# Optimization experiments

Measured on AMD Instinct MI355X. Metric: run time of the kernel, lower is better.

The kernel has to match this reference:

```python
import jax, jax.numpy as jnp
import numpy as np

ALPHA = 0.2  # LeakyReLU negative slope
NEG_INF = -1e12


def setup_inputs() -> dict:
    key = jax.random.key(0)
    k1, k2, k3, k4, k5 = jax.random.split(key, 5)
    N, F = 4096, 512
    inp = jax.random.normal(k1, (N, F), dtype=jnp.float32)
    adj = jax.random.randint(k2, (N, N), 0, 2).astype(jnp.float32)
    W = jax.random.normal(k3, (F, F), dtype=jnp.float32) * (1.414 / np.sqrt(F))
    a = jax.random.normal(k4, (2 * F, 1), dtype=jnp.float32) * 0.05
    wtrans = jax.random.normal(k5, (2 * F, F), dtype=jnp.float32) * (1.414 / np.sqrt(1.5 * F))
    return {"inp": inp, "adj": adj, "W": W, "a": a, "wtrans": wtrans}


def reference(inp, adj, W, a, wtrans):
    F_out = W.shape[1]
    h = inp @ W                                   # [N, F]
    Wh1 = h @ a[:F_out, :]                        # [N, 1]
    Wh2 = h @ a[F_out:, :]                        # [N, 1]
    e = jax.nn.leaky_relu(Wh1 + Wh2.T, ALPHA)     # [N, N]
    mask = adj > 0
    attention = jax.nn.softmax(jnp.where(mask, e, NEG_INF), axis=1)
    negative_attention = -jax.nn.softmax(jnp.where(mask, -e, NEG_INF), axis=1)
    # dropout p=0.0 (eval mode): identity
    h_prime = attention @ inp                     # [N, F_in]
    h_prime_negative = negative_attention @ inp   # [N, F_in]
    h_prime_double = jnp.concatenate([h_prime, h_prime_negative], axis=1)
    new_h_prime = h_prime_double @ wtrans         # [N, F_out]
    return jax.nn.elu(new_h_prime)
```

## Files before the change

### kernel.cpp

```cpp
#include <hip/hip_runtime.h>
#include <hip/hip_bf16.h>

#define N_NODES 4096
#define F_DIM   512
#define KTOT    8192
#define KSPLIT  8
#define LOG2E   1.44269504f

typedef __attribute__((ext_vector_type(8))) short bf16x8;
typedef __attribute__((ext_vector_type(4))) float f32x4;

__device__ inline unsigned short f2bf(float f) {
  union { float f; unsigned u; } c; c.f = f;
  unsigned r = c.u + 0x7fffu + ((c.u >> 16) & 1u);
  return (unsigned short)(r >> 16);
}
__device__ inline float bf2f(unsigned short u) {
  union { unsigned u; float f; } c; c.u = ((unsigned)u) << 16;
  return c.f;
}

__global__ void k_compute_v(const float* __restrict__ W, const float* __restrict__ a,
                            float* __restrict__ v1, float* __restrict__ v2) {
  int r = blockIdx.x, l = threadIdx.x;
  float s1 = 0.f, s2 = 0.f;
  for (int c = l; c < F_DIM; c += 64) {
    float w = W[(size_t)r * F_DIM + c];
    s1 += w * a[c];
    s2 += w * a[F_DIM + c];
  }
#pragma unroll
  for (int off = 32; off > 0; off >>= 1) { s1 += __shfl_down(s1, off); s2 += __shfl_down(s2, off); }
  if (l == 0) { v1[r] = s1; v2[r] = s2; }
}

__global__ void k_compute_wh(const float* __restrict__ inp, const float* __restrict__ v1,
                             const float* __restrict__ v2, float* __restrict__ Wh1,
                             float* __restrict__ Wh2) {
  int i = blockIdx.x, l = threadIdx.x;
  float s1 = 0.f, s2 = 0.f;
  for (int c = l; c < F_DIM; c += 64) {
    float x = inp[(size_t)i * F_DIM + c];
    s1 += x * v1[c];
    s2 += x * v2[c];
  }
#pragma unroll
  for (int off = 32; off > 0; off >>= 1) { s1 += __shfl_down(s1, off); s2 += __shfl_down(s2, off); }
  if (l == 0) { Wh1[i] = s1 * LOG2E; Wh2[i] = s2 * LOG2E; }
}

__global__ void k_transpose_bf16(const float* __restrict__ src, unsigned short* __restrict__ dst,
                                 int R, int C) {
  __shared__ float tile[32][33];
  int c0 = blockIdx.x * 32, r0 = blockIdx.y * 32;
  int tx = threadIdx.x, ty = threadIdx.y;
#pragma unroll
  for (int i = ty; i < 32; i += 8)
    tile[i][tx] = src[(size_t)(r0 + i) * C + c0 + tx];
  __syncthreads();
#pragma unroll
  for (int i = ty; i < 32; i += 8)
    dst[(size_t)(c0 + i) * R + r0 + tx] = f2bf(tile[tx][i]);
}

__global__ __launch_bounds__(256) void k_y(const float* __restrict__ inp,
                                           const unsigned short* __restrict__ wtT,
                                           unsigned short* __restrict__ YT) {
  int tid = threadIdx.x, l = tid & 63, w = tid >> 6;
  int row = l & 15, kg = l >> 4;
  int jt = blockIdx.x * 64 + w * 16;
  int cb = blockIdx.y * 64;
  f32x4 acc1[4] = {}, acc2[4] = {};
  const float* ap = inp + (size_t)(jt + row) * F_DIM + kg * 8;
  for (int k0 = 0; k0 < F_DIM; k0 += 32) {
    float4 f0 = *(const float4*)(ap + k0);
    float4 f1 = *(const float4*)(ap + k0 + 4);
    bf16x8 a;
    a[0] = (short)f2bf(f0.x); a[1] = (short)f2bf(f0.y); a[2] = (short)f2bf(f0.z); a[3] = (short)f2bf(f0.w);
    a[4] = (short)f2bf(f1.x); a[5] = (short)f2bf(f1.y); a[6] = (short)f2bf(f1.z); a[7] = (short)f2bf(f1.w);
#pragma unroll
    for (int n = 0; n < 4; n++) {
      const unsigned short* bp = wtT + (size_t)(cb + n * 16 + row) * 1024 + kg * 8 + k0;
      bf16x8 b1 = *(const bf16x8*)(bp);
      bf16x8 b2 = *(const bf16x8*)(bp + F_DIM);
      acc1[n] = __builtin_amdgcn_mfma_f32_16x16x32_bf16(a, b1, acc1[n], 0, 0, 0);
      acc2[n] = __builtin_amdgcn_mfma_f32_16x16x32_bf16(a, b2, acc2[n], 0, 0, 0);
    }
  }
  int jb = jt + kg * 4;
#pragma unroll
  for (int n = 0; n < 4; n++) {
    int f = cb + n * 16 + row;
    ushort4 o1, o2;
    o1.x = f2bf(acc1[n][0]); o1.y = f2bf(acc1[n][1]); o1.z = f2bf(acc1[n][2]); o1.w = f2bf(acc1[n][3]);
    o2.x = f2bf(acc2[n][0]); o2.y = f2bf(acc2[n][1]); o2.z = f2bf(acc2[n][2]); o2.w = f2bf(acc2[n][3]);
    *(ushort4*)(YT + (size_t)f * KTOT + jb) = o1;
    *(ushort4*)(YT + (size_t)f * KTOT + 4096 + jb) = o2;
  }
}

__global__ __launch_bounds__(256) void k_p(const float* __restrict__ adj,
                                           const float* __restrict__ Wh1,
                                           const float* __restrict__ Wh2,
                                           unsigned short* __restrict__ Pcat) {
  int i = blockIdx.x, t = threadIdx.x;
  float w1 = Wh1[i];
  int j0 = t * 16;
  const float* ar = adj + (size_t)i * N_NODES + j0;
  float4 A0 = *(const float4*)(ar);
  float4 A1 = *(const float4*)(ar + 4);
  float4 A2 = *(const float4*)(ar + 8);
  float4 A3 = *(const float4*)(ar + 12);
  float am[16] = {A0.x, A0.y, A0.z, A0.w, A1.x, A1.y, A1.z, A1.w,
                  A2.x, A2.y, A2.z, A2.w, A3.x, A3.y, A3.z, A3.w};
  float4 wv0 = *(const float4*)(Wh2 + j0);
  float4 wv1 = *(const float4*)(Wh2 + j0 + 4);
  float4 wv2 = *(const float4*)(Wh2 + j0 + 8);
  float4 wv3 = *(const float4*)(Wh2 + j0 + 12);
  float w2[16] = {wv0.x, wv0.y, wv0.z, wv0.w, wv1.x, wv1.y, wv1.z, wv1.w,
                  wv2.x, wv2.y, wv2.z, wv2.w, wv3.x, wv3.y, wv3.z, wv3.w};
  float pe[16], ne[16];
  float sp = 0.f, sn = 0.f;
#pragma unroll
  for (int r = 0; r < 16; r++) {
    float s = w1 + w2[r];
    float e = fmaxf(s, 0.2f * s);
    float p = exp2f(e);
    float n = exp2f(-e);
    if (!(am[r] > 0.f)) { p = 0.f; n = 0.f; }
    pe[r] = p; ne[r] = n; sp += p; sn += n;
  }
#pragma unroll
  for (int off = 1; off < 64; off <<= 1) { sp += __shfl_xor(sp, off); sn += __shfl_xor(sn, off); }
  __shared__ float red[2][4];
  int wv = t >> 6, ln = t & 63;
  if (ln == 0) { red[0][wv] = sp; red[1][wv] = sn; }
  __syncthreads();
  sp = red[0][0] + red[0][1] + red[0][2] + red[0][3];
  sn = red[1][0] + red[1][1] + red[1][2] + red[1][3];
  float rp = 1.f / sp;
  float rn = -1.f / sn;
  bf16x8 o;
#pragma unroll
  for (int r = 0; r < 8; r++) o[r] = (short)f2bf(pe[r] * rp);
  *(bf16x8*)(Pcat + (size_t)i * KTOT + j0) = o;
#pragma unroll
  for (int r = 0; r < 8; r++) o[r] = (short)f2bf(pe[8 + r] * rp);
  *(bf16x8*)(Pcat + (size_t)i * KTOT + j0 + 8) = o;
#pragma unroll
  for (int r = 0; r < 8; r++) o[r] = (short)f2bf(ne[r] * rn);
  *(bf16x8*)(Pcat + (size_t)i * KTOT + 4096 + j0) = o;
#pragma unroll
  for (int r = 0; r < 8; r++) o[r] = (short)f2bf(ne[8 + r] * rn);
  *(bf16x8*)(Pcat + (size_t)i * KTOT + 4096 + j0 + 8) = o;
}

#define GLOAD16(gp, lp) __builtin_amdgcn_global_load_lds( \
    (const __attribute__((address_space(1))) unsigned int*)(gp), \
    (__attribute__((address_space(3))) unsigned int*)(lp), 16, 0, 0)

__global__ __launch_bounds__(512, 2) void k_pv(const unsigned short* __restrict__ Pcat,
                                               const unsigned short* __restrict__ YT,
                                               unsigned short* __restrict__ part) {
  __shared__ unsigned short Ab[3][256 * 32];
  __shared__ unsigned short Bb[3][256 * 32];
  const int kchunk = KTOT / KSPLIT;
  int t = threadIdx.x;
  int l = t & 63, w = t >> 6;
  int la = l & 15, kg = l >> 4;
  int wr = w >> 2, wc = w & 3;
  int bm0 = blockIdx.x * 256, bn0 = blockIdx.y * 256;
  size_t kbase = (size_t)blockIdx.z * kchunk;
  const int nsteps = kchunk / 32;

  int seg = ((t & 3) ^ ((t >> 3) & 3)) << 4;
  const char* gA = (const char*)Pcat + ((size_t)(bm0 + (t >> 2)) * KTOT + kbase) * 2 + seg;
  const char* gB = (const char*)YT   + ((size_t)(bn0 + (t >> 2)) * KTOT + kbase) * 2 + seg;
  const size_t rstep = (size_t)128 * KTOT * 2;

  int aswz = (kg ^ ((la >> 1) & 3)) << 4;
  int abase = (wr * 128 + la) * 64 + aswz;
  int bbase = (wc * 64 + la) * 64 + aswz;

  f32x4 acc[8][4] = {};

#define STAGE3(buf, st) do { \
    const char* _ga = gA + (size_t)(st) * 64; \
    const char* _gb = gB + (size_t)(st) * 64; \
    char* _la = (char*)&Ab[buf][0] + w * 1024; \
    char* _lb = (char*)&Bb[buf][0] + w * 1024; \
    GLOAD16(_ga, _la); \
    GLOAD16(_ga + rstep, _la + 8192); \
    GLOAD16(_gb, _lb); \
    GLOAD16(_gb + rstep, _lb + 8192); \
  } while (0)

  STAGE3(0, 0);
  STAGE3(1, 1);
  for (int st = 0; st < nsteps; st++) {
    __builtin_amdgcn_s_barrier();
    int buf = st % 3;
    if (st + 2 < nsteps) {
      STAGE3((st + 2) % 3, st + 2);
      asm volatile("s_waitcnt vmcnt(8)" ::: "memory");
    } else if (st + 1 < nsteps) {
      asm volatile("s_waitcnt vmcnt(4)" ::: "memory");
    } else {
      asm volatile("s_waitcnt vmcnt(0)" ::: "memory");
    }
    __builtin_amdgcn_s_barrier();

    const char* Abp = (const char*)&Ab[buf][0];
    const char* Bbp = (const char*)&Bb[buf][0];
    bf16x8 af[8], bfr[4];
#pragma unroll
    for (int mi = 0; mi < 8; mi++) af[mi] = *(const bf16x8*)(Abp + abase + mi * 1024);
#pragma unroll
    for (int ni = 0; ni < 4; ni++) bfr[ni] = *(const bf16x8*)(Bbp + bbase + ni * 1024);
    __builtin_amdgcn_s_setprio(1);
#pragma unroll
    for (int mi = 0; mi < 8; mi++)
#pragma unroll
      for (int ni = 0; ni < 4; ni++)
        acc[mi][ni] = __builtin_amdgcn_mfma_f32_16x16x32_bf16(af[mi], bfr[ni], acc[mi][ni], 0, 0, 0);
    __builtin_amdgcn_s_setprio(0);
  }

  unsigned short* po = part + (size_t)blockIdx.z * (N_NODES * F_DIM);
#pragma unroll
  for (int mi = 0; mi < 8; mi++)
#pragma unroll
    for (int ni = 0; ni < 4; ni++)
#pragma unroll
      for (int r = 0; r < 4; r++) {
        int i_ = bm0 + wr * 128 + mi * 16 + kg * 4 + r;
        int f_ = bn0 + wc * 64 + ni * 16 + la;
        po[(size_t)i_ * F_DIM + f_] = f2bf(acc[mi][ni][r]);
      }
}

__global__ __launch_bounds__(256) void k_fin(const unsigned short* __restrict__ part,
                                             float* __restrict__ out) {
  size_t idx = ((size_t)blockIdx.x * 256 + threadIdx.x) * 8;
  float s[8] = {};
#pragma unroll
  for (int p = 0; p < KSPLIT; p++) {
    bf16x8 v = *(const bf16x8*)(part + (size_t)p * (N_NODES * F_DIM) + idx);
#pragma unroll
    for (int r = 0; r < 8; r++) s[r] += bf2f((unsigned short)v[r]);
  }
#pragma unroll
  for (int r = 0; r < 8; r++) s[r] = s[r] > 0.f ? s[r] : (__expf(s[r]) - 1.f);
  float4 o0 = make_float4(s[0], s[1], s[2], s[3]);
  float4 o1 = make_float4(s[4], s[5], s[6], s[7]);
  *(float4*)(out + idx) = o0;
  *(float4*)(out + idx + 4) = o1;
}

extern "C" void kernel_launch(void* const* d_in, const int* in_sizes, int n_in,
                              void* d_out, int out_size, void* d_ws, size_t ws_size,
                              hipStream_t stream) {
  (void)in_sizes; (void)n_in; (void)out_size; (void)ws_size;
  const float* inp    = (const float*)d_in[0];
  const float* adj    = (const float*)d_in[1];
  const float* W      = (const float*)d_in[2];
  const float* a      = (const float*)d_in[3];
  const float* wtrans = (const float*)d_in[4];
  float* out = (float*)d_out;

  char* ws = (char*)d_ws;
  float* v1  = (float*)ws;
  float* v2  = (float*)(ws + 2048);
  float* Wh1 = (float*)(ws + 4096);
  float* Wh2 = (float*)(ws + 20480);

  const size_t PSZ = (size_t)N_NODES * F_DIM * 2;
  char* regA = ws + 65536;
  unsigned short* wtT  = (unsigned short*)regA;
  unsigned short* part = (unsigned short*)regA;
  unsigned short* YT   = (unsigned short*)(regA + KSPLIT * PSZ);
  unsigned short* Pcat = (unsigned short*)(regA + KSPLIT * PSZ + 8388608);

  k_compute_v<<<512, 64, 0, stream>>>(W, a, v1, v2);
  k_compute_wh<<<4096, 64, 0, stream>>>(inp, v1, v2, Wh1, Wh2);
  k_transpose_bf16<<<dim3(16, 32), dim3(32, 8), 0, stream>>>(wtrans, wtT, 1024, F_DIM);
  k_y<<<dim3(64, 8), 256, 0, stream>>>(inp, wtT, YT);
  k_p<<<4096, 256, 0, stream>>>(adj, Wh1, Wh2, Pcat);
  k_pv<<<dim3(16, 2, KSPLIT), 512, 0, stream>>>(Pcat, YT, part);
  k_fin<<<1024, 256, 0, stream>>>(part, out);
}
```

Measured before the change: 130.1 us.

## Generate attention probabilities on the fly inside PV GEMM from packed mask bits

The softmax kernel no longer materializes the bf16 Pcat matrix (4096x8192). It writes only the per-row reciprocal sums and a 16-bit-per-thread packed adjacency mask. The PV GEMM kernel recomputes exp of the LeakyReLU scores from Wh1/Wh2 and the mask bits directly into its LDS A-buffer, while B tiles stream through a triple buffer. This removes the 64MB write and reread of P in exchange for redundant exp work inside the GEMM, done once per column block, plus more LDS use that may reduce occupancy.

```diff
diff --git a/kernel.cpp b/kernel.cpp
--- a/kernel.cpp
+++ b/kernel.cpp
@@ -5,6 +5,7 @@
 #define F_DIM   512
 #define KTOT    8192
 #define KSPLIT  8
+#define NSTEPS  32
 #define LOG2E   1.44269504f
 
 typedef __attribute__((ext_vector_type(8))) short bf16x8;
@@ -99,10 +100,11 @@
   }
 }
 
-__global__ __launch_bounds__(256) void k_p(const float* __restrict__ adj,
-                                           const float* __restrict__ Wh1,
-                                           const float* __restrict__ Wh2,
-                                           unsigned short* __restrict__ Pcat) {
+__global__ __launch_bounds__(256) void k_sums(const float* __restrict__ adj,
+                                              const float* __restrict__ Wh1,
+                                              const float* __restrict__ Wh2,
+                                              float* __restrict__ rp, float* __restrict__ rn,
+                                              unsigned short* __restrict__ mbits) {
   int i = blockIdx.x, t = threadIdx.x;
   float w1 = Wh1[i];
   int j0 = t * 16;
@@ -119,99 +121,136 @@
   float4 wv3 = *(const float4*)(Wh2 + j0 + 12);
   float w2[16] = {wv0.x, wv0.y, wv0.z, wv0.w, wv1.x, wv1.y, wv1.z, wv1.w,
                   wv2.x, wv2.y, wv2.z, wv2.w, wv3.x, wv3.y, wv3.z, wv3.w};
-  float pe[16], ne[16];
   float sp = 0.f, sn = 0.f;
+  unsigned mask = 0;
 #pragma unroll
   for (int r = 0; r < 16; r++) {
     float s = w1 + w2[r];
     float e = fmaxf(s, 0.2f * s);
     float p = exp2f(e);
     float n = exp2f(-e);
-    if (!(am[r] > 0.f)) { p = 0.f; n = 0.f; }
-    pe[r] = p; ne[r] = n; sp += p; sn += n;
-  }
+    bool con = am[r] > 0.f;
+    if (con) mask |= (1u << r); else { p = 0.f; n = 0.f; }
+    sp += p; sn += n;
+  }
+  mbits[(size_t)i * 256 + t] = (unsigned short)mask;
 #pragma unroll
   for (int off = 1; off < 64; off <<= 1) { sp += __shfl_xor(sp, off); sn += __shfl_xor(sn, off); }
   __shared__ float red[2][4];
   int wv = t >> 6, ln = t & 63;
   if (ln == 0) { red[0][wv] = sp; red[1][wv] = sn; }
   __syncthreads();
-  sp = red[0][0] + red[0][1] + red[0][2] + red[0][3];
-  sn = red[1][0] + red[1][1] + red[1][2] + red[1][3];
-  float rp = 1.f / sp;
-  float rn = -1.f / sn;
-  bf16x8 o;
-#pragma unroll
-  for (int r = 0; r < 8; r++) o[r] = (short)f2bf(pe[r] * rp);
-  *(bf16x8*)(Pcat + (size_t)i * KTOT + j0) = o;
-#pragma unroll
-  for (int r = 0; r < 8; r++) o[r] = (short)f2bf(pe[8 + r] * rp);
-  *(bf16x8*)(Pcat + (size_t)i * KTOT + j0 + 8) = o;
-#pragma unroll
-  for (int r = 0; r < 8; r++) o[r] = (short)f2bf(ne[r] * rn);
-  *(bf16x8*)(Pcat + (size_t)i * KTOT + 4096 + j0) = o;
-#pragma unroll
-  for (int r = 0; r < 8; r++) o[r] = (short)f2bf(ne[8 + r] * rn);
-  *(bf16x8*)(Pcat + (size_t)i * KTOT + 4096 + j0 + 8) = o;
+  if (t == 0) {
+    sp = red[0][0] + red[0][1] + red[0][2] + red[0][3];
+    sn = red[1][0] + red[1][1] + red[1][2] + red[1][3];
+    rp[i] = 1.f / sp;
+    rn[i] = -1.f / sn;
+  }
 }
 
 #define GLOAD16(gp, lp) __builtin_amdgcn_global_load_lds( \
     (const __attribute__((address_space(1))) unsigned int*)(gp), \
     (__attribute__((address_space(3))) unsigned int*)(lp), 16, 0, 0)
 
-__global__ __launch_bounds__(512, 2) void k_pv(const unsigned short* __restrict__ Pcat,
-                                               const unsigned short* __restrict__ YT,
-                                               unsigned short* __restrict__ part) {
-  __shared__ unsigned short Ab[3][256 * 32];
+__global__ __launch_bounds__(512, 2) void k_pv(
+    const unsigned short* __restrict__ YT, const unsigned short* __restrict__ mbits,
+    const float* __restrict__ Wh1L, const float* __restrict__ Wh2L,
+    const float* __restrict__ rp, const float* __restrict__ rn,
+    unsigned short* __restrict__ part) {
+  __shared__ unsigned short Ab[2][256 * 32];
   __shared__ unsigned short Bb[3][256 * 32];
-  const int kchunk = KTOT / KSPLIT;
+  __shared__ float swh2[1024];
+  __shared__ unsigned short sbit[256 * 66];
   int t = threadIdx.x;
   int l = t & 63, w = t >> 6;
   int la = l & 15, kg = l >> 4;
   int wr = w >> 2, wc = w & 3;
   int bm0 = blockIdx.x * 256, bn0 = blockIdx.y * 256;
-  size_t kbase = (size_t)blockIdx.z * kchunk;
-  const int nsteps = kchunk / 32;
+  int z = blockIdx.z;
+  size_t kbase = (size_t)z * (KTOT / KSPLIT);
+  int jbase = (z & 3) * 1024;
+  bool neg = z >= 4;
 
   int seg = ((t & 3) ^ ((t >> 3) & 3)) << 4;
-  const char* gA = (const char*)Pcat + ((size_t)(bm0 + (t >> 2)) * KTOT + kbase) * 2 + seg;
-  const char* gB = (const char*)YT   + ((size_t)(bn0 + (t >> 2)) * KTOT + kbase) * 2 + seg;
+  const char* gB = (const char*)YT + ((size_t)(bn0 + (t >> 2)) * KTOT + kbase) * 2 + seg;
   const size_t rstep = (size_t)128 * KTOT * 2;
 
   int aswz = (kg ^ ((la >> 1) & 3)) << 4;
   int abase = (wr * 128 + la) * 64 + aswz;
   int bbase = (wc * 64 + la) * 64 + aswz;
 
-  f32x4 acc[8][4] = {};
-
-#define STAGE3(buf, st) do { \
-    const char* _ga = gA + (size_t)(st) * 64; \
+  int r = t >> 1, h = t & 1;
+  {
+    const uint4* src = (const uint4*)(mbits + (size_t)(bm0 + r) * 256 + (z & 3) * 64 + h * 32);
+    unsigned short* dst = &sbit[r * 66 + h * 32];
+#pragma unroll
+    for (int q = 0; q < 4; q++) {
+      uint4 v = src[q];
+      *(unsigned*)(dst + q * 8 + 0) = v.x;
+      *(unsigned*)(dst + q * 8 + 2) = v.y;
+      *(unsigned*)(dst + q * 8 + 4) = v.z;
+      *(unsigned*)(dst + q * 8 + 6) = v.w;
+    }
+  }
+  if (t < 256) *(float4*)&swh2[t * 4] = *(const float4*)(Wh2L + jbase + t * 4);
+  float w1 = Wh1L[bm0 + r];
+  float fac = neg ? rn[bm0 + r] : rp[bm0 + r];
+  float sgn = neg ? -1.f : 1.f;
+  int xk = (r >> 1) & 3;
+  char* abrow0 = (char*)&Ab[0][0] + r * 64;
+  char* abrow1 = (char*)&Ab[1][0] + r * 64;
+  int ps0 = ((2 * h) ^ xk) * 16, ps1 = ((2 * h + 1) ^ xk) * 16;
+
+  auto genP = [&](int gs) {
+    int koff = gs * 32 + h * 16;
+    unsigned mb = sbit[r * 66 + gs * 2 + h];
+    bf16x8 o0, o1;
+#pragma unroll
+    for (int e = 0; e < 8; e++) {
+      float s1 = w1 + swh2[koff + e];
+      float e1 = fmaxf(s1, 0.2f * s1);
+      float p1 = exp2f(sgn * e1);
+      p1 = ((mb >> e) & 1u) ? p1 * fac : 0.f;
+      o0[e] = (short)f2bf(p1);
+      float s2 = w1 + swh2[koff + 8 + e];
+      float e2 = fmaxf(s2, 0.2f * s2);
+      float p2 = exp2f(sgn * e2);
+      p2 = ((mb >> (8 + e)) & 1u) ? p2 * fac : 0.f;
+      o1[e] = (short)f2bf(p2);
+    }
+    char* ab = (gs & 1) ? abrow1 : abrow0;
+    *(bf16x8*)(ab + ps0) = o0;
+    *(bf16x8*)(ab + ps1) = o1;
+  };
+
+#define STAGE_B(buf, st) do { \
     const char* _gb = gB + (size_t)(st) * 64; \
-    char* _la = (char*)&Ab[buf][0] + w * 1024; \
     char* _lb = (char*)&Bb[buf][0] + w * 1024; \
-    GLOAD16(_ga, _la); \
-    GLOAD16(_ga + rstep, _la + 8192); \
     GLOAD16(_gb, _lb); \
     GLOAD16(_gb + rstep, _lb + 8192); \
   } while (0)
 
-  STAGE3(0, 0);
-  STAGE3(1, 1);
-  for (int st = 0; st < nsteps; st++) {
+  f32x4 acc[8][4] = {};
+
+  STAGE_B(0, 0);
+  STAGE_B(1, 1);
+  asm volatile("s_waitcnt lgkmcnt(0)" ::: "memory");
+  __builtin_amdgcn_s_barrier();
+  genP(0);
+
+  int b_st = 0, b_nx = 2;
+  for (int st = 0; st < NSTEPS; st++) {
     __builtin_amdgcn_s_barrier();
-    int buf = st % 3;
-    if (st + 2 < nsteps) {
-      STAGE3((st + 2) % 3, st + 2);
-      asm volatile("s_waitcnt vmcnt(8)" ::: "memory");
-    } else if (st + 1 < nsteps) {
-      asm volatile("s_waitcnt vmcnt(4)" ::: "memory");
-    } else {
-      asm volatile("s_waitcnt vmcnt(0)" ::: "memory");
-    }
+    if (st + 2 < NSTEPS) STAGE_B(b_nx, st + 2);
+    if (st + 1 < NSTEPS) genP(st + 1);
+    asm volatile("s_waitcnt lgkmcnt(0)" ::: "memory");
+    if (st + 2 < NSTEPS)      asm volatile("s_waitcnt vmcnt(4)" ::: "memory");
+    else if (st + 1 < NSTEPS) asm volatile("s_waitcnt vmcnt(2)" ::: "memory");
+    else                      asm volatile("s_waitcnt vmcnt(0)" ::: "memory");
     __builtin_amdgcn_s_barrier();
 
-    const char* Abp = (const char*)&Ab[buf][0];
-    const char* Bbp = (const char*)&Bb[buf][0];
+    const char* Abp = (const char*)&Ab[st & 1][0];
+    const char* Bbp = (const char*)&Bb[b_st][0];
     bf16x8 af[8], bfr[4];
 #pragma unroll
     for (int mi = 0; mi < 8; mi++) af[mi] = *(const bf16x8*)(Abp + abase + mi * 1024);
@@ -224,18 +263,20 @@
       for (int ni = 0; ni < 4; ni++)
         acc[mi][ni] = __builtin_amdgcn_mfma_f32_16x16x32_bf16(af[mi], bfr[ni], acc[mi][ni], 0, 0, 0);
     __builtin_amdgcn_s_setprio(0);
-  }
-
-  unsigned short* po = part + (size_t)blockIdx.z * (N_NODES * F_DIM);
+    b_st = (b_st + 1 == 3) ? 0 : b_st + 1;
+    b_nx = (b_nx + 1 == 3) ? 0 : b_nx + 1;
+  }
+
+  unsigned short* po = part + (size_t)z * (N_NODES * F_DIM);
 #pragma unroll
   for (int mi = 0; mi < 8; mi++)
 #pragma unroll
     for (int ni = 0; ni < 4; ni++)
 #pragma unroll
-      for (int r = 0; r < 4; r++) {
-        int i_ = bm0 + wr * 128 + mi * 16 + kg * 4 + r;
+      for (int q = 0; q < 4; q++) {
+        int i_ = bm0 + wr * 128 + mi * 16 + kg * 4 + q;
         int f_ = bn0 + wc * 64 + ni * 16 + la;
-        po[(size_t)i_ * F_DIM + f_] = f2bf(acc[mi][ni][r]);
+        po[(size_t)i_ * F_DIM + f_] = f2bf(acc[mi][ni][q]);
       }
 }
 
@@ -247,10 +288,10 @@
   for (int p = 0; p < KSPLIT; p++) {
     bf16x8 v = *(const bf16x8*)(part + (size_t)p * (N_NODES * F_DIM) + idx);
 #pragma unroll
-    for (int r = 0; r < 8; r++) s[r] += bf2f((unsigned short)v[r]);
-  }
-#pragma unroll
-  for (int r = 0; r < 8; r++) s[r] = s[r] > 0.f ? s[r] : (__expf(s[r]) - 1.f);
+    for (int q = 0; q < 8; q++) s[q] += bf2f((unsigned short)v[q]);
+  }
+#pragma unroll
+  for (int q = 0; q < 8; q++) s[q] = s[q] > 0.f ? s[q] : (__expf(s[q]) - 1.f);
   float4 o0 = make_float4(s[0], s[1], s[2], s[3]);
   float4 o1 = make_float4(s[4], s[5], s[6], s[7]);
   *(float4*)(out + idx) = o0;
@@ -273,19 +314,18 @@
   float* v2  = (float*)(ws + 2048);
   float* Wh1 = (float*)(ws + 4096);
   float* Wh2 = (float*)(ws + 20480);
-
-  const size_t PSZ = (size_t)N_NODES * F_DIM * 2;
-  char* regA = ws + 65536;
-  unsigned short* wtT  = (unsigned short*)regA;
-  unsigned short* part = (unsigned short*)regA;
-  unsigned short* YT   = (unsigned short*)(regA + KSPLIT * PSZ);
-  unsigned short* Pcat = (unsigned short*)(regA + KSPLIT * PSZ + 8388608);
+  float* rp  = (float*)(ws + 36864);
+  float* rn  = (float*)(ws + 53248);
+  unsigned short* mbits = (unsigned short*)(ws + 69632);
+  unsigned short* wtT   = (unsigned short*)(ws + 69632 + 2097152);
+  unsigned short* YT    = (unsigned short*)(ws + 69632 + 3145728);
+  unsigned short* part  = (unsigned short*)(ws + 69632 + 11534336);
 
   k_compute_v<<<512, 64, 0, stream>>>(W, a, v1, v2);
   k_compute_wh<<<4096, 64, 0, stream>>>(inp, v1, v2, Wh1, Wh2);
   k_transpose_bf16<<<dim3(16, 32), dim3(32, 8), 0, stream>>>(wtrans, wtT, 1024, F_DIM);
   k_y<<<dim3(64, 8), 256, 0, stream>>>(inp, wtT, YT);
-  k_p<<<4096, 256, 0, stream>>>(adj, Wh1, Wh2, Pcat);
-  k_pv<<<dim3(16, 2, KSPLIT), 512, 0, stream>>>(Pcat, YT, part);
+  k_sums<<<4096, 256, 0, stream>>>(adj, Wh1, Wh2, rp, rn, mbits);
+  k_pv<<<dim3(16, 2, KSPLIT), 512, 0, stream>>>(YT, mbits, Wh1, Wh2, rp, rn, part);
   k_fin<<<1024, 256, 0, stream>>>(part, out);
 }
```

Result: slower. 150.8 us (+15.8%).

## Store attention matrix in pre-tiled panel layout for contiguous GEMM A-loads

Applied to the files above, without the earlier changes.

The softmax kernel now writes Pcat in a blocked layout. Each k-split chunk is arranged as 256-row panels made of 32-column slabs, so every 256x32 tile the PV GEMM needs is one contiguous 16 KB region. The GEMM's A-operand loads become fully sequential streams instead of rows strided by 16 KB, which is meant to improve DRAM and TLB efficiency. The cost is scattered 16-byte writes in the producer kernel, and the layout is tied to the fixed problem dimensions.

```diff
diff --git a/kernel.cpp b/kernel.cpp
--- a/kernel.cpp
+++ b/kernel.cpp
@@ -5,7 +5,12 @@
 #define F_DIM   512
 #define KTOT    8192
 #define KSPLIT  8
+#define NSTEPS  32
 #define LOG2E   1.44269504f
+
+#define SLAB_E   8192ull
+#define PANEL_E  262144ull
+#define ZBLK_E   4194304ull
 
 typedef __attribute__((ext_vector_type(8))) short bf16x8;
 typedef __attribute__((ext_vector_type(4))) float f32x4;
@@ -140,19 +145,24 @@
   sn = red[1][0] + red[1][1] + red[1][2] + red[1][3];
   float rp = 1.f / sp;
   float rn = -1.f / sn;
+
+  int zz = j0 >> 10;
+  int local = j0 & 1023;
+  size_t base = (size_t)zz * ZBLK_E + (size_t)(i >> 8) * PANEL_E
+              + (size_t)(local >> 5) * SLAB_E + (size_t)(i & 255) * 32 + (local & 31);
   bf16x8 o;
 #pragma unroll
   for (int r = 0; r < 8; r++) o[r] = (short)f2bf(pe[r] * rp);
-  *(bf16x8*)(Pcat + (size_t)i * KTOT + j0) = o;
+  *(bf16x8*)(Pcat + base) = o;
 #pragma unroll
   for (int r = 0; r < 8; r++) o[r] = (short)f2bf(pe[8 + r] * rp);
-  *(bf16x8*)(Pcat + (size_t)i * KTOT + j0 + 8) = o;
+  *(bf16x8*)(Pcat + base + 8) = o;
 #pragma unroll
   for (int r = 0; r < 8; r++) o[r] = (short)f2bf(ne[r] * rn);
-  *(bf16x8*)(Pcat + (size_t)i * KTOT + 4096 + j0) = o;
+  *(bf16x8*)(Pcat + base + 4 * ZBLK_E) = o;
 #pragma unroll
   for (int r = 0; r < 8; r++) o[r] = (short)f2bf(ne[8 + r] * rn);
-  *(bf16x8*)(Pcat + (size_t)i * KTOT + 4096 + j0 + 8) = o;
+  *(bf16x8*)(Pcat + base + 4 * ZBLK_E + 8) = o;
 }
 
 #define GLOAD16(gp, lp) __builtin_amdgcn_global_load_lds( \
@@ -164,19 +174,19 @@
                                                unsigned short* __restrict__ part) {
   __shared__ unsigned short Ab[3][256 * 32];
   __shared__ unsigned short Bb[3][256 * 32];
-  const int kchunk = KTOT / KSPLIT;
   int t = threadIdx.x;
   int l = t & 63, w = t >> 6;
   int la = l & 15, kg = l >> 4;
   int wr = w >> 2, wc = w & 3;
   int bm0 = blockIdx.x * 256, bn0 = blockIdx.y * 256;
-  size_t kbase = (size_t)blockIdx.z * kchunk;
-  const int nsteps = kchunk / 32;
+  int z = blockIdx.z;
+  size_t kbase = (size_t)z * (KTOT / KSPLIT);
 
   int seg = ((t & 3) ^ ((t >> 3) & 3)) << 4;
-  const char* gA = (const char*)Pcat + ((size_t)(bm0 + (t >> 2)) * KTOT + kbase) * 2 + seg;
-  const char* gB = (const char*)YT   + ((size_t)(bn0 + (t >> 2)) * KTOT + kbase) * 2 + seg;
-  const size_t rstep = (size_t)128 * KTOT * 2;
+  const char* gA = (const char*)(Pcat + ((size_t)z * 16 + blockIdx.x) * PANEL_E)
+                 + (t >> 2) * 64 + seg;
+  const char* gB = (const char*)YT + ((size_t)(bn0 + (t >> 2)) * KTOT + kbase) * 2 + seg;
+  const size_t rstepB = (size_t)128 * KTOT * 2;
 
   int aswz = (kg ^ ((la >> 1) & 3)) << 4;
   int abase = (wr * 128 + la) * 64 + aswz;
@@ -185,25 +195,25 @@
   f32x4 acc[8][4] = {};
 
 #define STAGE3(buf, st) do { \
-    const char* _ga = gA + (size_t)(st) * 64; \
+    const char* _ga = gA + (size_t)(st) * 16384; \
     const char* _gb = gB + (size_t)(st) * 64; \
     char* _la = (char*)&Ab[buf][0] + w * 1024; \
     char* _lb = (char*)&Bb[buf][0] + w * 1024; \
     GLOAD16(_ga, _la); \
-    GLOAD16(_ga + rstep, _la + 8192); \
+    GLOAD16(_ga + 8192, _la + 8192); \
     GLOAD16(_gb, _lb); \
-    GLOAD16(_gb + rstep, _lb + 8192); \
+    GLOAD16(_gb + rstepB, _lb + 8192); \
   } while (0)
 
   STAGE3(0, 0);
   STAGE3(1, 1);
-  for (int st = 0; st < nsteps; st++) {
+  for (int st = 0; st < NSTEPS; st++) {
     __builtin_amdgcn_s_barrier();
     int buf = st % 3;
-    if (st + 2 < nsteps) {
+    if (st + 2 < NSTEPS) {
       STAGE3((st + 2) % 3, st + 2);
       asm volatile("s_waitcnt vmcnt(8)" ::: "memory");
-    } else if (st + 1 < nsteps) {
+    } else if (st + 1 < NSTEPS) {
       asm volatile("s_waitcnt vmcnt(4)" ::: "memory");
     } else {
       asm volatile("s_waitcnt vmcnt(0)" ::: "memory");
@@ -226,16 +236,16 @@
     __builtin_amdgcn_s_setprio(0);
   }
 
-  unsigned short* po = part + (size_t)blockIdx.z * (N_NODES * F_DIM);
+  unsigned short* po = part + (size_t)z * (N_NODES * F_DIM);
 #pragma unroll
   for (int mi = 0; mi < 8; mi++)
 #pragma unroll
     for (int ni = 0; ni < 4; ni++)
 #pragma unroll
-      for (int r = 0; r < 4; r++) {
-        int i_ = bm0 + wr * 128 + mi * 16 + kg * 4 + r;
+      for (int q = 0; q < 4; q++) {
+        int i_ = bm0 + wr * 128 + mi * 16 + kg * 4 + q;
         int f_ = bn0 + wc * 64 + ni * 16 + la;
-        po[(size_t)i_ * F_DIM + f_] = f2bf(acc[mi][ni][r]);
+        po[(size_t)i_ * F_DIM + f_] = f2bf(acc[mi][ni][q]);
       }
 }
 
@@ -247,10 +257,10 @@
   for (int p = 0; p < KSPLIT; p++) {
     bf16x8 v = *(const bf16x8*)(part + (size_t)p * (N_NODES * F_DIM) + idx);
 #pragma unroll
-    for (int r = 0; r < 8; r++) s[r] += bf2f((unsigned short)v[r]);
-  }
-#pragma unroll
-  for (int r = 0; r < 8; r++) s[r] = s[r] > 0.f ? s[r] : (__expf(s[r]) - 1.f);
+    for (int q = 0; q < 8; q++) s[q] += bf2f((unsigned short)v[q]);
+  }
+#pragma unroll
+  for (int q = 0; q < 8; q++) s[q] = s[q] > 0.f ? s[q] : (__expf(s[q]) - 1.f);
   float4 o0 = make_float4(s[0], s[1], s[2], s[3]);
   float4 o1 = make_float4(s[4], s[5], s[6], s[7]);
   *(float4*)(out + idx) = o0;
```

New measurement: 132.4 us. Within noise of the previous version (+1.7%).

## Restructure PV GEMM into 8-phase ping-pong schedule with 64-wide K tiles

Applied to the files above, without the earlier changes.

The split-K PV GEMM kernel now uses 64-deep K tiles in a double-buffered 128 KB LDS layout with an 8-way XOR swizzle. Each tile's MFMA work is split into eight phases, and global-to-LDS loads for upcoming tiles are interleaved between phases with explicit barriers and waitcnts. The aim is better overlap of memory traffic with MFMA work and fewer barriers per FLOP. In exchange, occupancy drops to one block per CU (launch bounds 512,1), and the hand-tuned vmcnt accounting is fragile.

```diff
diff --git a/kernel.cpp b/kernel.cpp
--- a/kernel.cpp
+++ b/kernel.cpp
@@ -159,84 +159,90 @@
     (const __attribute__((address_space(1))) unsigned int*)(gp), \
     (__attribute__((address_space(3))) unsigned int*)(lp), 16, 0, 0)
 
-__global__ __launch_bounds__(512, 2) void k_pv(const unsigned short* __restrict__ Pcat,
+__global__ __launch_bounds__(512, 1) void k_pv(const unsigned short* __restrict__ Pcat,
                                                const unsigned short* __restrict__ YT,
                                                unsigned short* __restrict__ part) {
-  __shared__ unsigned short Ab[3][256 * 32];
-  __shared__ unsigned short Bb[3][256 * 32];
-  const int kchunk = KTOT / KSPLIT;
+  __shared__ char ldsA[65536];
+  __shared__ char ldsB[65536];
   int t = threadIdx.x;
   int l = t & 63, w = t >> 6;
   int la = l & 15, kg = l >> 4;
   int wr = w >> 2, wc = w & 3;
   int bm0 = blockIdx.x * 256, bn0 = blockIdx.y * 256;
-  size_t kbase = (size_t)blockIdx.z * kchunk;
-  const int nsteps = kchunk / 32;
-
-  int seg = ((t & 3) ^ ((t >> 3) & 3)) << 4;
-  const char* gA = (const char*)Pcat + ((size_t)(bm0 + (t >> 2)) * KTOT + kbase) * 2 + seg;
-  const char* gB = (const char*)YT   + ((size_t)(bn0 + (t >> 2)) * KTOT + kbase) * 2 + seg;
-  const size_t rstep = (size_t)128 * KTOT * 2;
-
-  int aswz = (kg ^ ((la >> 1) & 3)) << 4;
-  int abase = (wr * 128 + la) * 64 + aswz;
-  int bbase = (wc * 64 + la) * 64 + aswz;
+  int z = blockIdx.z;
+  size_t zoffB = (size_t)z * (KTOT / KSPLIT) * 2;
+
+  int lgq = ((t & 7) ^ ((t >> 3) & 7)) << 4;
+  const char* gPc = (const char*)Pcat + (size_t)(bm0 + (t >> 3)) * (KTOT * 2) + zoffB + lgq;
+  const char* gYt = (const char*)YT  + (size_t)(bn0 + (t >> 3)) * (KTOT * 2) + zoffB + lgq;
+
+#define STA(T, q) GLOAD16(gPc + (size_t)(q) * 64 * (KTOT * 2) + (size_t)(T) * 128, \
+                          ldsA + ((T) & 1) * 32768 + ((q) >> 1) * 16384 + ((q) & 1) * 8192 + w * 1024)
+#define STB(T, u) GLOAD16(gYt + (size_t)(u) * 64 * (KTOT * 2) + (size_t)(T) * 128, \
+                          ldsB + ((T) & 1) * 32768 + ((u) >> 1) * 16384 + ((u) & 1) * 8192 + w * 1024)
 
   f32x4 acc[8][4] = {};
-
-#define STAGE3(buf, st) do { \
-    const char* _ga = gA + (size_t)(st) * 64; \
-    const char* _gb = gB + (size_t)(st) * 64; \
-    char* _la = (char*)&Ab[buf][0] + w * 1024; \
-    char* _lb = (char*)&Bb[buf][0] + w * 1024; \
-    GLOAD16(_ga, _la); \
-    GLOAD16(_ga + rstep, _la + 8192); \
-    GLOAD16(_gb, _lb); \
-    GLOAD16(_gb + rstep, _lb + 8192); \
-  } while (0)
-
-  STAGE3(0, 0);
-  STAGE3(1, 1);
-  for (int st = 0; st < nsteps; st++) {
-    __builtin_amdgcn_s_barrier();
-    int buf = st % 3;
-    if (st + 2 < nsteps) {
-      STAGE3((st + 2) % 3, st + 2);
-      asm volatile("s_waitcnt vmcnt(8)" ::: "memory");
-    } else if (st + 1 < nsteps) {
-      asm volatile("s_waitcnt vmcnt(4)" ::: "memory");
-    } else {
-      asm volatile("s_waitcnt vmcnt(0)" ::: "memory");
-    }
-    __builtin_amdgcn_s_barrier();
-
-    const char* Abp = (const char*)&Ab[buf][0];
-    const char* Bbp = (const char*)&Bb[buf][0];
-    bf16x8 af[8], bfr[4];
-#pragma unroll
-    for (int mi = 0; mi < 8; mi++) af[mi] = *(const bf16x8*)(Abp + abase + mi * 1024);
-#pragma unroll
-    for (int ni = 0; ni < 4; ni++) bfr[ni] = *(const bf16x8*)(Bbp + bbase + ni * 1024);
-    __builtin_amdgcn_s_setprio(1);
-#pragma unroll
-    for (int mi = 0; mi < 8; mi++)
+  bf16x8 af[4], bfr[2][4];
+
+#define PHASE(D, RH, KS, READB, STAGES, VMC) do { \
+  const char* Ah_ = ldsA + (D) * 32768 + wr * 16384 + (RH) * 64 * 128; \
+  _Pragma("unroll") for (int mi = 0; mi < 4; mi++) \
+    af[mi] = *(const bf16x8*)(Ah_ + (mi * 16 + la) * 128 + ((((KS) * 4 + kg)) ^ (la & 7)) * 16); \
+  if (READB) { \
+    const char* Bh_ = ldsB + (D) * 32768 + (wc >> 1) * 16384; \
+    _Pragma("unroll") for (int ni = 0; ni < 4; ni++) \
+      bfr[KS][ni] = *(const bf16x8*)(Bh_ + ((wc & 1) * 64 + ni * 16 + la) * 128 + ((((KS) * 4 + kg)) ^ (la & 7)) * 16); \
+  } \
+  STAGES; \
+  VMC; \
+  __builtin_amdgcn_s_barrier(); \
+  asm volatile("s_waitcnt lgkmcnt(0)" ::: "memory"); \
+  __builtin_amdgcn_sched_barrier(0); \
+  __builtin_amdgcn_s_setprio(1); \
+  _Pragma("unroll") for (int mi = 0; mi < 4; mi++) \
+    _Pragma("unroll") for (int ni = 0; ni < 4; ni++) \
+      acc[(RH) * 4 + mi][ni] = __builtin_amdgcn_mfma_f32_16x16x32_bf16(af[mi], bfr[KS][ni], acc[(RH) * 4 + mi][ni], 0, 0, 0); \
+  __builtin_amdgcn_s_setprio(0); \
+  __builtin_amdgcn_s_barrier(); \
+} while (0)
+
+  STA(0, 0); STA(0, 1); STA(0, 2); STA(0, 3);
+  STB(0, 0); STB(0, 1); STB(0, 2); STB(0, 3);
+  STA(1, 0); STA(1, 1); STA(1, 2); STA(1, 3);
+  STB(1, 0); STB(1, 1); STB(1, 2); STB(1, 3);
+  asm volatile("s_waitcnt vmcnt(8)" ::: "memory");
+  __builtin_amdgcn_s_barrier();
+
+  for (int it = 0; it < 8; ++it) {
+    int T1 = 2 * it + 1, T2 = 2 * it + 2, T3 = 2 * it + 3;
+    bool mid = (it > 0), more = (it < 7);
+    PHASE(0, 0, 0, true,  { if (mid) { STA(T1, 1); STA(T1, 3); } }, {});
+    PHASE(0, 0, 1, true,  { if (mid) { STB(T1, 0); STB(T1, 1); } }, {});
+    PHASE(0, 1, 0, false, { if (mid) { STB(T1, 2); STB(T1, 3); } }, {});
+    PHASE(0, 1, 1, false, { if (more) { STA(T2, 0); STA(T2, 2); } },
+          { if (more) asm volatile("s_waitcnt vmcnt(2)" ::: "memory");
+            else      asm volatile("s_waitcnt vmcnt(0)" ::: "memory"); });
+    PHASE(1, 0, 0, true,  { if (more) { STA(T2, 1); STA(T2, 3); } }, {});
+    PHASE(1, 0, 1, true,  { if (more) { STB(T2, 0); STB(T2, 1); } }, {});
+    PHASE(1, 1, 0, false, { if (more) { STB(T2, 2); STB(T2, 3); } }, {});
+    PHASE(1, 1, 1, false, { if (more) { STA(T3, 0); STA(T3, 2); } },
+          { if (more) asm volatile("s_waitcnt vmcnt(2)" ::: "memory");
+            else      asm volatile("s_waitcnt vmcnt(0)" ::: "memory"); });
+  }
+
+  unsigned short* po = part + (size_t)z * (N_NODES * F_DIM);
+#pragma unroll
+  for (int rh = 0; rh < 2; rh++)
+#pragma unroll
+    for (int mi = 0; mi < 4; mi++)
 #pragma unroll
       for (int ni = 0; ni < 4; ni++)
-        acc[mi][ni] = __builtin_amdgcn_mfma_f32_16x16x32_bf16(af[mi], bfr[ni], acc[mi][ni], 0, 0, 0);
-    __builtin_amdgcn_s_setprio(0);
-  }
-
-  unsigned short* po = part + (size_t)blockIdx.z * (N_NODES * F_DIM);
-#pragma unroll
-  for (int mi = 0; mi < 8; mi++)
-#pragma unroll
-    for (int ni = 0; ni < 4; ni++)
-#pragma unroll
-      for (int r = 0; r < 4; r++) {
-        int i_ = bm0 + wr * 128 + mi * 16 + kg * 4 + r;
-        int f_ = bn0 + wc * 64 + ni * 16 + la;
-        po[(size_t)i_ * F_DIM + f_] = f2bf(acc[mi][ni][r]);
-      }
+#pragma unroll
+        for (int q = 0; q < 4; q++) {
+          int i_ = bm0 + wr * 128 + rh * 64 + mi * 16 + kg * 4 + q;
+          int f_ = bn0 + wc * 64 + ni * 16 + la;
+          po[(size_t)i_ * F_DIM + f_] = f2bf(acc[rh * 4 + mi][ni][q]);
+        }
 }
 
 __global__ __launch_bounds__(256) void k_fin(const unsigned short* __restrict__ part,
@@ -247,10 +253,10 @@
   for (int p = 0; p < KSPLIT; p++) {
     bf16x8 v = *(const bf16x8*)(part + (size_t)p * (N_NODES * F_DIM) + idx);
 #pragma unroll
-    for (int r = 0; r < 8; r++) s[r] += bf2f((unsigned short)v[r]);
-  }
-#pragma unroll
-  for (int r = 0; r < 8; r++) s[r] = s[r] > 0.f ? s[r] : (__expf(s[r]) - 1.f);
+    for (int q = 0; q < 8; q++) s[q] += bf2f((unsigned short)v[q]);
+  }
+#pragma unroll
+  for (int q = 0; q < 8; q++) s[q] = s[q] > 0.f ? s[q] : (__expf(s[q]) - 1.f);
   float4 o0 = make_float4(s[0], s[1], s[2], s[3]);
   float4 o1 = make_float4(s[4], s[5], s[6], s[7]);
   *(float4*)(out + idx) = o0;
```

Result: faster. 122.5 us (-5.9%).
